# Optimization experiments

Hardware: AMD Instinct MI355X
Metric: run time of the kernel (lower is better)

Reference implementation:

```python
import jax, jax.numpy as jnp
import numpy as np

EMB = 1024
HID = 1536
NE = 8


def setup_inputs() -> dict:
    key = jax.random.key(0)
    ks = jax.random.split(key, 8)
    B, N, E, H, ne = 4, 2048, EMB, HID, NE
    s = 1.0 / np.sqrt(E)
    sh = 1.0 / np.sqrt(H)
    return {
        "x": jax.random.normal(ks[0], (B, N, E), dtype=jnp.float32),
        "Wr": jax.random.uniform(ks[1], (E, ne), minval=-s, maxval=s, dtype=jnp.float32),
        "br": jax.random.uniform(ks[2], (ne,), minval=-s, maxval=s, dtype=jnp.float32),
        "W1": jax.random.uniform(ks[3], (ne, E, H), minval=-s, maxval=s, dtype=jnp.float32),
        "b1": jax.random.uniform(ks[4], (ne, H), minval=-s, maxval=s, dtype=jnp.float32),
        "W2": jax.random.uniform(ks[5], (ne, H, E), minval=-sh, maxval=sh, dtype=jnp.float32),
        "b2": jax.random.uniform(ks[6], (ne, E), minval=-sh, maxval=sh, dtype=jnp.float32),
        "k": 2,
    }


def reference(x, Wr, br, W1, b1, W2, b2, k):
    B, N, E = x.shape
    T = B * N
    ne = Wr.shape[1]
    flat = x.reshape(T, E)
    logits = flat @ Wr + br                      # [T, ne]
    _, topk_idx = jax.lax.top_k(logits, k)       # [T, k]
    # counts[t, e] = number of top-k slots of token t assigned to expert e
    counts = jax.nn.one_hot(topk_idx, ne, dtype=flat.dtype).sum(axis=1)  # [T, ne]
    out = jnp.zeros_like(flat)
    for e in range(ne):  # small fixed loop over experts (structurally distinct weights)
        h = jax.nn.gelu(flat @ W1[e] + b1[e], approximate=False)  # torch nn.GELU = exact erf
        y = h @ W2[e] + b2[e]
        out = out + counts[:, e:e + 1] * y
    out = out / k
    return out.reshape(B, N, E)
```

## Files before the change

### kernel.cpp

```cpp
#include <hip/hip_runtime.h>
#include <hip/hip_bf16.h>
#include <math.h>

#define T_TOK 8192
#define EMB   1024
#define HID   1536
#define NE    8
#define NBINB 64
#define BINTOK (T_TOK / NBINB)

typedef float  floatx4 __attribute__((ext_vector_type(4)));
typedef __bf16 bf16x8  __attribute__((ext_vector_type(8)));

#define WS_COUNTS   0
#define WS_OFFSETS  1024
#define WS_FLAGS    2048
#define WS_BHIST    4096
#define WS_TOKMAP   8192
#define WS_TOKLIST  270336
#define WS_YBUF     532480
#define WS_W1T      34086912
#define WS_W2T      59252736
#define WS_H        84418560
#define WS_NEEDED   135143424

__device__ __forceinline__ float eload(const void* p, size_t idx, bool f32) {
  return f32 ? ((const float*)p)[idx] : (float)(((const __bf16*)p)[idx]);
}

__device__ __forceinline__ void glds16(const void* g, void* l) {
  __builtin_amdgcn_global_load_lds(
      (const __attribute__((address_space(1))) unsigned int*)g,
      (__attribute__((address_space(3))) unsigned int*)l, 16, 0, 0);
}

__global__ __launch_bounds__(256)
void sniff_kernel(const void* p0, const void* p1, const void* p2, const void* p3,
                  const void* p4, const void* p5, const void* p6, int* flags) {
  const void* ps[7] = {p0, p1, p2, p3, p4, p5, p6};
  const int nelem[7] = {T_TOK * EMB, EMB * NE, NE, NE * EMB * HID, NE * HID, NE * HID * EMB, NE * EMB};
  int t = blockIdx.x;
  const unsigned* w = (const unsigned*)ps[t];
  int nw = nelem[t] / 2;
  if (nw > 2048) nw = 2048;
  __shared__ int s_pl, s_nz;
  if (threadIdx.x == 0) { s_pl = 0; s_nz = 0; }
  __syncthreads();
  int pl = 0, nz = 0;
  for (int i = threadIdx.x; i < nw; i += 256) {
    unsigned v = w[i];
    if (v == 0) continue;
    nz++;
    unsigned e = (v >> 23) & 0xFF;
    if (e >= 100 && e <= 150) pl++;
  }
  atomicAdd(&s_pl, pl);
  atomicAdd(&s_nz, nz);
  __syncthreads();
  if (threadIdx.x == 0) flags[t] = (2 * s_pl > s_nz) ? 1 : 0;
}

__global__ __launch_bounds__(256)
void logits_kernel(const void* __restrict__ x, const void* __restrict__ Wr,
                   const void* __restrict__ br, const int* __restrict__ kptr,
                   const int* __restrict__ flags, int* __restrict__ topk,
                   __bf16* __restrict__ xbf) {
  const bool xf32  = flags[0] != 0;
  const bool wrf32 = flags[1] != 0;
  const bool brf32 = flags[2] != 0;
  const int wave = threadIdx.x >> 6;
  const int lane = threadIdx.x & 63;
  const int t = blockIdx.x * 4 + wave;

  float xv[16];
  {
    size_t base = (size_t)t * EMB + lane * 16;
    if (xf32) {
      const float* g = (const float*)x + base;
#pragma unroll
      for (int j = 0; j < 16; ++j) xv[j] = g[j];
    } else {
      bf16x8 u = *(const bf16x8*)((const __bf16*)x + base);
      bf16x8 v = *(const bf16x8*)((const __bf16*)x + base + 8);
#pragma unroll
      for (int j = 0; j < 8; ++j) { xv[j] = (float)u[j]; xv[8 + j] = (float)v[j]; }
    }
  }
  {
    bf16x8 o0, o1;
#pragma unroll
    for (int j = 0; j < 8; ++j) { o0[j] = (__bf16)xv[j]; o1[j] = (__bf16)xv[8 + j]; }
    __bf16* xo = xbf + (size_t)t * EMB + lane * 16;
    *(bf16x8*)xo = o0;
    *(bf16x8*)(xo + 8) = o1;
  }
  float acc[NE];
#pragma unroll
  for (int e = 0; e < NE; ++e) acc[e] = 0.f;
  if (wrf32) {
#pragma unroll
    for (int j = 0; j < 16; ++j) {
      const float* wr = (const float*)Wr + (size_t)(lane * 16 + j) * NE;
#pragma unroll
      for (int e = 0; e < NE; ++e) acc[e] += xv[j] * wr[e];
    }
  } else {
#pragma unroll
    for (int j = 0; j < 16; ++j) {
      bf16x8 wr = *(const bf16x8*)((const __bf16*)Wr + (size_t)(lane * 16 + j) * NE);
#pragma unroll
      for (int e = 0; e < NE; ++e) acc[e] += xv[j] * (float)wr[e];
    }
  }
#pragma unroll
  for (int e = 0; e < NE; ++e) {
#pragma unroll
    for (int off = 32; off > 0; off >>= 1)
      acc[e] += __shfl_xor(acc[e], off, 64);
  }
  if (lane == 0) {
    int k = kptr[0];
    if (k < 1) k = 1; if (k > NE) k = NE;
    float lg[NE];
#pragma unroll
    for (int e = 0; e < NE; ++e) lg[e] = acc[e] + eload(br, e, brf32);
    for (int s = 0; s < k; ++s) {
      int bi = 0; float bv = lg[0];
#pragma unroll
      for (int e = 1; e < NE; ++e) { if (lg[e] > bv) { bv = lg[e]; bi = e; } }
      lg[bi] = -3.0e38f;
      topk[t * 8 + s] = bi;
    }
  }
}

__global__ __launch_bounds__(128)
void bin1_kernel(const int* __restrict__ topk, const int* __restrict__ kptr,
                 int* __restrict__ bhist) {
  __shared__ int lhist[NE];
  if (threadIdx.x < NE) lhist[threadIdx.x] = 0;
  __syncthreads();
  int k = kptr[0];
  if (k < 1) k = 1; if (k > NE) k = NE;
  const int t = blockIdx.x * BINTOK + threadIdx.x;
  for (int s = 0; s < k; ++s) atomicAdd(&lhist[topk[t * 8 + s] & 7], 1);
  __syncthreads();
  if (threadIdx.x < NE) bhist[blockIdx.x * NE + threadIdx.x] = lhist[threadIdx.x];
}

__global__ __launch_bounds__(256)
void scan_kernel(int* __restrict__ bhist, int* __restrict__ counts, int* __restrict__ offsets) {
  __shared__ int sh[NBINB * NE];
  __shared__ int scnt[NE];
  __shared__ int soff[NE + 1];
  const int tid = threadIdx.x;
  for (int i = tid; i < NBINB * NE; i += 256) sh[i] = bhist[i];
  __syncthreads();
  if (tid < NE) {
    int s = 0;
    for (int b = 0; b < NBINB; ++b) s += sh[b * NE + tid];
    scnt[tid] = s;
  }
  __syncthreads();
  if (tid == 0) {
    int s = 0;
    for (int e = 0; e < NE; ++e) { soff[e] = s; s += scnt[e]; }
    soff[NE] = s;
  }
  __syncthreads();
  if (tid < NE) {
    int run = soff[tid];
    for (int b = 0; b < NBINB; ++b) {
      int v = sh[b * NE + tid];
      sh[b * NE + tid] = run;
      run += v;
    }
  }
  __syncthreads();
  for (int i = tid; i < NBINB * NE; i += 256) bhist[i] = sh[i];
  if (tid < NE) counts[tid] = scnt[tid];
  if (tid < NE + 1) offsets[tid] = soff[tid];
}

__global__ __launch_bounds__(128)
void bin2_kernel(const int* __restrict__ bhist, const int* __restrict__ offsets,
                 const int* __restrict__ kptr,
                 int* __restrict__ tok_list, int* __restrict__ tokmap) {
  __shared__ int lbase[NE];
  __shared__ int lcnt[NE];
  if (threadIdx.x < NE) {
    lbase[threadIdx.x] = bhist[blockIdx.x * NE + threadIdx.x];
    lcnt[threadIdx.x] = 0;
  }
  __syncthreads();
  int k = kptr[0];
  if (k < 1) k = 1; if (k > NE) k = NE;
  const int t = blockIdx.x * BINTOK + threadIdx.x;
  for (int s = 0; s < k; ++s) {
    int e = tokmap[t * 8 + s] & 7;
    int pos = atomicAdd(&lcnt[e], 1);
    int grow = lbase[e] + pos;
    tok_list[e * T_TOK + (grow - offsets[e])] = t;
    tokmap[t * 8 + s] = (e << 16) | grow;
  }
}

__global__ __launch_bounds__(256)
void transpose_kernel(const void* __restrict__ in, __bf16* __restrict__ out, int K, int N,
                      const int* __restrict__ flags, int fidx) {
  const bool f32 = flags[fidx] != 0;
  __shared__ __bf16 tile[64][65];
  size_t eoff = (size_t)blockIdx.z * (size_t)K * (size_t)N;
  int n0 = blockIdx.x * 64;
  int k0 = blockIdx.y * 64;
  int tx = threadIdx.x & 63;
  int ty = threadIdx.x >> 6;
#pragma unroll
  for (int i = 0; i < 16; ++i) {
    int r = i * 4 + ty;
    tile[r][tx] = (__bf16)eload(in, eoff + (size_t)(k0 + r) * N + (n0 + tx), f32);
  }
  __syncthreads();
#pragma unroll
  for (int i = 0; i < 16; ++i) {
    int r = i * 4 + ty;
    out[eoff + (size_t)(n0 + r) * K + (k0 + tx)] = tile[tx][r];
  }
}


#define STAGE3(SL, KO) do {                                              \
    __bf16* _d = lds + (SL) * 12288 + wave * 512;                        \
    glds16(pA0 + (KO), _d);                                              \
    glds16(pB0 + (KO), _d + 4096);                                       \
    glds16(pB1 + (KO), _d + 8192);                                       \
  } while (0)

#define KBODY(SL, DOSTAGE, TT) do {                                      \
    const char* _s = (const char*)lds + (SL) * 24576;                    \
    bf16x8 _af[4], _bf[4];                                               \
    _Pragma("unroll")                                                    \
    for (int _i = 0; _i < 4; ++_i) _af[_i] = *(const bf16x8*)(_s + aOff[_i]); \
    _Pragma("unroll")                                                    \
    for (int _j = 0; _j < 4; ++_j) _bf[_j] = *(const bf16x8*)(_s + bOff[_j]); \
    if (DOSTAGE) { int _sl2 = (SL) == 0 ? 2 : (SL) - 1;                  \
                   STAGE3(_sl2, (size_t)((TT) + 2) * 32); }              \
    __builtin_amdgcn_s_setprio(1);                                       \
    _Pragma("unroll")                                                    \
    for (int _i = 0; _i < 4; ++_i)                                       \
      _Pragma("unroll")                                                  \
      for (int _j = 0; _j < 4; ++_j)                                     \
        acc[_i][_j] = __builtin_amdgcn_mfma_f32_16x16x32_bf16(_af[_i], _bf[_j], acc[_i][_j], 0, 0, 0); \
    __builtin_amdgcn_s_setprio(0);                                       \
  } while (0)

__global__ __launch_bounds__(512, 4)
void gemm1_kernel(const __bf16* __restrict__ xbf, const __bf16* __restrict__ w1t,
                  const void* __restrict__ b1, const int* __restrict__ counts,
                  const int* __restrict__ offsets, const int* __restrict__ tok_list,
                  const int* __restrict__ flags, __bf16* __restrict__ hbuf) {
  const int flat = blockIdx.x;
  const int e   = flat & 7;
  const int idx = flat >> 3;
  const int g   = idx / 6;
  const int nT  = idx % 6;
  const int cnt = counts[e];
  const bool b1f32 = flags[4] != 0;

  __shared__ __align__(16) __bf16 lds[3 * 12288];

  const int wave = threadIdx.x >> 6;
  const int lane = threadIdx.x & 63;
  const int sr = wave * 16 + (lane >> 2);
  const int cg = (lane & 3) ^ ((sr >> 1) & 3);

  const __bf16* pB0 = w1t + ((size_t)e * HID + nT * 256 + sr) * EMB + cg * 8;
  const __bf16* pB1 = w1t + ((size_t)e * HID + nT * 256 + 128 + sr) * EMB + cg * 8;

  const int wm = (wave >> 2) * 64;
  const int wn = (wave & 3) * 64;
  const int fr = lane & 15;
  const int fc = lane >> 4;
  int aOff[4], bOff[4];
#pragma unroll
  for (int i = 0; i < 4; ++i) { int R = wm + i * 16 + fr; aOff[i] = R * 64 + ((fc ^ ((R >> 1) & 3)) << 4); }
#pragma unroll
  for (int j = 0; j < 4; ++j) { int R = wn + j * 16 + fr; bOff[j] = 8192 + R * 64 + ((fc ^ ((R >> 1) & 3)) << 4); }

  const int colBase = nT * 256 + wn + fr;
  float bv[4];
#pragma unroll
  for (int j = 0; j < 4; ++j) bv[j] = eload(b1, (size_t)e * HID + colBase + j * 16, b1f32);

  for (int mT = g; mT * 128 < cnt; mT += 16) {
    const int tokA = tok_list[e * T_TOK + mT * 128 + sr];
    const __bf16* pA0 = xbf + (size_t)tokA * EMB + cg * 8;

    floatx4 acc[4][4];
#pragma unroll
    for (int i = 0; i < 4; ++i)
#pragma unroll
      for (int j = 0; j < 4; ++j) acc[i][j] = (floatx4){0.f, 0.f, 0.f, 0.f};

    __syncthreads();
    STAGE3(0, 0); STAGE3(1, 32);
    int sl = 0;
    for (int t = 0; t < 31; ++t) {
      asm volatile("s_waitcnt vmcnt(3)" ::: "memory");
      __builtin_amdgcn_s_barrier();
      KBODY(sl, (t + 2 < 32), t);
      sl = (sl + 1 == 3) ? 0 : sl + 1;
    }
    asm volatile("s_waitcnt vmcnt(0)" ::: "memory");
    __builtin_amdgcn_s_barrier();
    KBODY(sl, 0, 0);

    const int hBase = offsets[e] + mT * 128;
#pragma unroll
    for (int i = 0; i < 4; ++i) {
      const int rowLoc = wm + i * 16 + fc * 4;
#pragma unroll
      for (int r = 0; r < 4; ++r) {
        const int row = rowLoc + r;
        if (mT * 128 + row < cnt) {
          __bf16* hp = hbuf + (size_t)(hBase + row) * HID + colBase;
#pragma unroll
          for (int j = 0; j < 4; ++j) {
            float v = acc[i][j][r] + bv[j];
            float gl = 0.5f * v * (1.0f + erff(v * 0.70710678118654752f));
            hp[j * 16] = (__bf16)gl;
          }
        }
      }
    }
  }
}

__global__ __launch_bounds__(512, 4)
void gemm2_kernel(const __bf16* __restrict__ hbuf, const __bf16* __restrict__ w2t,
                  const void* __restrict__ b2, const int* __restrict__ counts,
                  const int* __restrict__ offsets, const int* __restrict__ flags,
                  __bf16* __restrict__ ybuf) {
  const int flat = blockIdx.x;
  const int e   = flat & 7;
  const int idx = flat >> 3;
  const int g   = idx >> 2;
  const int nT  = idx & 3;
  const int cnt = counts[e];
  const bool b2f32 = flags[6] != 0;

  __shared__ __align__(16) __bf16 lds[3 * 12288];

  const int wave = threadIdx.x >> 6;
  const int lane = threadIdx.x & 63;
  const int sr = wave * 16 + (lane >> 2);
  const int cg = (lane & 3) ^ ((sr >> 1) & 3);

  const __bf16* pB0 = w2t + ((size_t)e * EMB + nT * 256 + sr) * HID + cg * 8;
  const __bf16* pB1 = w2t + ((size_t)e * EMB + nT * 256 + 128 + sr) * HID + cg * 8;

  const int wm = (wave >> 2) * 64;
  const int wn = (wave & 3) * 64;
  const int fr = lane & 15;
  const int fc = lane >> 4;
  int aOff[4], bOff[4];
#pragma unroll
  for (int i = 0; i < 4; ++i) { int R = wm + i * 16 + fr; aOff[i] = R * 64 + ((fc ^ ((R >> 1) & 3)) << 4); }
#pragma unroll
  for (int j = 0; j < 4; ++j) { int R = wn + j * 16 + fr; bOff[j] = 8192 + R * 64 + ((fc ^ ((R >> 1) & 3)) << 4); }

  const int colBase = nT * 256 + wn + fr;
  float bv[4];
#pragma unroll
  for (int j = 0; j < 4; ++j) bv[j] = eload(b2, (size_t)e * EMB + colBase + j * 16, b2f32);

  const int lastRow = offsets[NE] - 1;

  for (int mT = g; mT * 128 < cnt; mT += 16) {
    const int rowBase = offsets[e] + mT * 128;
    const int rA = min(rowBase + sr, lastRow);
    const __bf16* pA0 = hbuf + (size_t)rA * HID + cg * 8;

    floatx4 acc[4][4];
#pragma unroll
    for (int i = 0; i < 4; ++i)
#pragma unroll
      for (int j = 0; j < 4; ++j) acc[i][j] = (floatx4){0.f, 0.f, 0.f, 0.f};

    __syncthreads();
    STAGE3(0, 0); STAGE3(1, 32);
    int sl = 0;
    for (int t = 0; t < 47; ++t) {
      asm volatile("s_waitcnt vmcnt(3)" ::: "memory");
      __builtin_amdgcn_s_barrier();
      KBODY(sl, (t + 2 < 48), t);
      sl = (sl + 1 == 3) ? 0 : sl + 1;
    }
    asm volatile("s_waitcnt vmcnt(0)" ::: "memory");
    __builtin_amdgcn_s_barrier();
    KBODY(sl, 0, 0);

#pragma unroll
    for (int i = 0; i < 4; ++i) {
      const int rowLoc = wm + i * 16 + fc * 4;
#pragma unroll
      for (int r = 0; r < 4; ++r) {
        const int row = rowLoc + r;
        if (mT * 128 + row < cnt) {
          __bf16* yp = ybuf + (size_t)(rowBase + row) * EMB + colBase;
#pragma unroll
          for (int j = 0; j < 4; ++j)
            yp[j * 16] = (__bf16)(acc[i][j][r] + bv[j]);
        }
      }
    }
  }
}

__global__ __launch_bounds__(256)
void combine_kernel(const __bf16* __restrict__ ybuf, const int* __restrict__ tokmap,
                    const int* __restrict__ kptr, const int* __restrict__ flags,
                    void* __restrict__ out) {
  const bool f32 = flags[0] != 0;
  const int wave = threadIdx.x >> 6;
  const int lane = threadIdx.x & 63;
  const int t = blockIdx.x * 4 + wave;
  int k = kptr[0];
  if (k < 1) k = 1; if (k > NE) k = NE;
  const float invk = 1.0f / (float)k;
  int rows[NE];
  for (int s = 0; s < k; ++s) rows[s] = tokmap[t * 8 + s] & 0xFFFF;
#pragma unroll
  for (int c = 0; c < 2; ++c) {
    const int i = c * 512 + lane * 8;
    float a[8];
#pragma unroll
    for (int j = 0; j < 8; ++j) a[j] = 0.f;
    for (int s = 0; s < k; ++s) {
      bf16x8 y = *(const bf16x8*)(ybuf + (size_t)rows[s] * EMB + i);
#pragma unroll
      for (int j = 0; j < 8; ++j) a[j] += (float)y[j];
    }
    if (f32) {
      float* op = (float*)out + (size_t)t * EMB + i;
      float4 u = {a[0] * invk, a[1] * invk, a[2] * invk, a[3] * invk};
      float4 v = {a[4] * invk, a[5] * invk, a[6] * invk, a[7] * invk};
      *(float4*)op = u;
      *(float4*)(op + 4) = v;
    } else {
      bf16x8 o;
#pragma unroll
      for (int j = 0; j < 8; ++j) o[j] = (__bf16)(a[j] * invk);
      *(bf16x8*)((__bf16*)out + (size_t)t * EMB + i) = o;
    }
  }
}

extern "C" void kernel_launch(void* const* d_in, const int* in_sizes, int n_in,
                              void* d_out, int out_size, void* d_ws, size_t ws_size,
                              hipStream_t stream) {
  (void)in_sizes; (void)n_in; (void)out_size;
  if (ws_size < (size_t)WS_NEEDED) return;

  const void* x  = d_in[0];
  const void* Wr = d_in[1];
  const void* br = d_in[2];
  const void* W1 = d_in[3];
  const void* b1 = d_in[4];
  const void* W2 = d_in[5];
  const void* b2 = d_in[6];
  const int* kptr = (const int*)d_in[7];

  char* ws = (char*)d_ws;
  int*    counts   = (int*)(ws + WS_COUNTS);
  int*    offsets  = (int*)(ws + WS_OFFSETS);
  int*    flags    = (int*)(ws + WS_FLAGS);
  int*    bhist    = (int*)(ws + WS_BHIST);
  int*    tokmap   = (int*)(ws + WS_TOKMAP);
  int*    tok_list = (int*)(ws + WS_TOKLIST);
  __bf16* ybuf     = (__bf16*)(ws + WS_YBUF);
  __bf16* xbf      = (__bf16*)(ws + WS_YBUF);
  __bf16* w1t      = (__bf16*)(ws + WS_W1T);
  __bf16* w2t      = (__bf16*)(ws + WS_W2T);
  __bf16* hbuf     = (__bf16*)(ws + WS_H);

  hipMemsetAsync(ws, 0, WS_YBUF, stream);

  sniff_kernel<<<dim3(7), 256, 0, stream>>>(x, Wr, br, W1, b1, W2, b2, flags);

  transpose_kernel<<<dim3(HID / 64, EMB / 64, NE), 256, 0, stream>>>(W1, w1t, EMB, HID, flags, 3);
  transpose_kernel<<<dim3(EMB / 64, HID / 64, NE), 256, 0, stream>>>(W2, w2t, HID, EMB, flags, 5);

  logits_kernel<<<dim3(T_TOK / 4), 256, 0, stream>>>(x, Wr, br, kptr, flags, tokmap, xbf);
  bin1_kernel<<<dim3(NBINB), 128, 0, stream>>>(tokmap, kptr, bhist);
  scan_kernel<<<dim3(1), 256, 0, stream>>>(bhist, counts, offsets);
  bin2_kernel<<<dim3(NBINB), 128, 0, stream>>>(bhist, offsets, kptr, tok_list, tokmap);

  gemm1_kernel<<<dim3(8 * 16 * 6), 512, 0, stream>>>(
      xbf, w1t, b1, counts, offsets, tok_list, flags, hbuf);
  gemm2_kernel<<<dim3(8 * 16 * 4), 512, 0, stream>>>(
      hbuf, w2t, b2, counts, offsets, flags, ybuf);

  combine_kernel<<<dim3(T_TOK / 4), 256, 0, stream>>>(ybuf, tokmap, kptr, flags, d_out);
}
```

Baseline: 441.0 us.

## Replace pipelined 128x256 GEMM tiles with simple single-buffer 128x128 tiles

Both expert GEMMs drop the 3-stage LDS pipeline with 512-thread 128x256 tiles and use 256-thread 128x128 tiles that load and compute one K-slice per iteration between two barriers, doubling the grid. The two weight transposes are merged into one launch, and the memset shrinks to only the token list. The change loses load/compute overlap and halves the weight reuse per tile. gemm2 also drops the row clamp on A loads.

```diff
diff --git a/kernel.cpp b/kernel.cpp
--- a/kernel.cpp
+++ b/kernel.cpp
@@ -206,11 +206,16 @@
 }
 
 __global__ __launch_bounds__(256)
-void transpose_kernel(const void* __restrict__ in, __bf16* __restrict__ out, int K, int N,
-                      const int* __restrict__ flags, int fidx) {
-  const bool f32 = flags[fidx] != 0;
+void transpose2_kernel(const void* __restrict__ W1, const void* __restrict__ W2,
+                       __bf16* __restrict__ w1t, __bf16* __restrict__ w2t,
+                       const int* __restrict__ flags) {
+  const int z = blockIdx.z;
+  const void* in; __bf16* out; int K, N; bool f32;
+  if (z < 8) { in = W1; out = w1t; K = EMB; N = HID; f32 = flags[3] != 0; }
+  else       { in = W2; out = w2t; K = HID; N = EMB; f32 = flags[5] != 0; }
+  if ((int)blockIdx.x * 64 >= N || (int)blockIdx.y * 64 >= K) return;
   __shared__ __bf16 tile[64][65];
-  size_t eoff = (size_t)blockIdx.z * (size_t)K * (size_t)N;
+  size_t eoff = (size_t)(z & 7) * (size_t)K * (size_t)N;
   int n0 = blockIdx.x * 64;
   int k0 = blockIdx.y * 64;
   int tx = threadIdx.x & 63;
@@ -229,32 +234,7 @@
 }
 
 
-#define STAGE3(SL, KO) do {                                              \
-    __bf16* _d = lds + (SL) * 12288 + wave * 512;                        \
-    glds16(pA0 + (KO), _d);                                              \
-    glds16(pB0 + (KO), _d + 4096);                                       \
-    glds16(pB1 + (KO), _d + 8192);                                       \
-  } while (0)
-
-#define KBODY(SL, DOSTAGE, TT) do {                                      \
-    const char* _s = (const char*)lds + (SL) * 24576;                    \
-    bf16x8 _af[4], _bf[4];                                               \
-    _Pragma("unroll")                                                    \
-    for (int _i = 0; _i < 4; ++_i) _af[_i] = *(const bf16x8*)(_s + aOff[_i]); \
-    _Pragma("unroll")                                                    \
-    for (int _j = 0; _j < 4; ++_j) _bf[_j] = *(const bf16x8*)(_s + bOff[_j]); \
-    if (DOSTAGE) { int _sl2 = (SL) == 0 ? 2 : (SL) - 1;                  \
-                   STAGE3(_sl2, (size_t)((TT) + 2) * 32); }              \
-    __builtin_amdgcn_s_setprio(1);                                       \
-    _Pragma("unroll")                                                    \
-    for (int _i = 0; _i < 4; ++_i)                                       \
-      _Pragma("unroll")                                                  \
-      for (int _j = 0; _j < 4; ++_j)                                     \
-        acc[_i][_j] = __builtin_amdgcn_mfma_f32_16x16x32_bf16(_af[_i], _bf[_j], acc[_i][_j], 0, 0, 0); \
-    __builtin_amdgcn_s_setprio(0);                                       \
-  } while (0)
-
-__global__ __launch_bounds__(512, 4)
+__global__ __launch_bounds__(256, 4)
 void gemm1_kernel(const __bf16* __restrict__ xbf, const __bf16* __restrict__ w1t,
                   const void* __restrict__ b1, const int* __restrict__ counts,
                   const int* __restrict__ offsets, const int* __restrict__ tok_list,
@@ -262,39 +242,51 @@
   const int flat = blockIdx.x;
   const int e   = flat & 7;
   const int idx = flat >> 3;
-  const int g   = idx / 6;
-  const int nT  = idx % 6;
+  const int g   = idx / 12;
+  const int nT  = idx % 12;
   const int cnt = counts[e];
   const bool b1f32 = flags[4] != 0;
 
-  __shared__ __align__(16) __bf16 lds[3 * 12288];
+  __shared__ __align__(16) __bf16 As[128 * 32];
+  __shared__ __align__(16) __bf16 Bs[128 * 32];
 
   const int wave = threadIdx.x >> 6;
   const int lane = threadIdx.x & 63;
-  const int sr = wave * 16 + (lane >> 2);
-  const int cg = (lane & 3) ^ ((sr >> 1) & 3);
-
-  const __bf16* pB0 = w1t + ((size_t)e * HID + nT * 256 + sr) * EMB + cg * 8;
-  const __bf16* pB1 = w1t + ((size_t)e * HID + nT * 256 + 128 + sr) * EMB + cg * 8;
-
-  const int wm = (wave >> 2) * 64;
-  const int wn = (wave & 3) * 64;
+  const int sr = lane >> 2;
+  const int r0 = wave * 16 + sr;
+  const int r1 = 64 + wave * 16 + sr;
+  const int cg = (lane & 3) ^ ((r0 >> 1) & 3);
+
+  const __bf16* pB0base = w1t + ((size_t)e * HID + nT * 128 + r0) * EMB + cg * 8;
+  const __bf16* pB1base = w1t + ((size_t)e * HID + nT * 128 + r1) * EMB + cg * 8;
+
+  __bf16* dA0 = As + wave * 512;
+  __bf16* dA1 = As + 2048 + wave * 512;
+  __bf16* dB0 = Bs + wave * 512;
+  __bf16* dB1 = Bs + 2048 + wave * 512;
+
+  const int wm = (wave & 1) * 64;
+  const int wn = (wave >> 1) * 64;
   const int fr = lane & 15;
   const int fc = lane >> 4;
   int aOff[4], bOff[4];
 #pragma unroll
   for (int i = 0; i < 4; ++i) { int R = wm + i * 16 + fr; aOff[i] = R * 64 + ((fc ^ ((R >> 1) & 3)) << 4); }
 #pragma unroll
-  for (int j = 0; j < 4; ++j) { int R = wn + j * 16 + fr; bOff[j] = 8192 + R * 64 + ((fc ^ ((R >> 1) & 3)) << 4); }
-
-  const int colBase = nT * 256 + wn + fr;
+  for (int j = 0; j < 4; ++j) { int R = wn + j * 16 + fr; bOff[j] = R * 64 + ((fc ^ ((R >> 1) & 3)) << 4); }
+
+  const int colBase = nT * 128 + wn + fr;
   float bv[4];
 #pragma unroll
   for (int j = 0; j < 4; ++j) bv[j] = eload(b1, (size_t)e * HID + colBase + j * 16, b1f32);
 
   for (int mT = g; mT * 128 < cnt; mT += 16) {
-    const int tokA = tok_list[e * T_TOK + mT * 128 + sr];
-    const __bf16* pA0 = xbf + (size_t)tokA * EMB + cg * 8;
+    const int tokA0 = tok_list[e * T_TOK + mT * 128 + r0];
+    const int tokA1 = tok_list[e * T_TOK + mT * 128 + r1];
+    const __bf16* pA0 = xbf + (size_t)tokA0 * EMB + cg * 8;
+    const __bf16* pA1 = xbf + (size_t)tokA1 * EMB + cg * 8;
+    const __bf16* pB0 = pB0base;
+    const __bf16* pB1 = pB1base;
 
     floatx4 acc[4][4];
 #pragma unroll
@@ -302,18 +294,23 @@
 #pragma unroll
       for (int j = 0; j < 4; ++j) acc[i][j] = (floatx4){0.f, 0.f, 0.f, 0.f};
 
-    __syncthreads();
-    STAGE3(0, 0); STAGE3(1, 32);
-    int sl = 0;
-    for (int t = 0; t < 31; ++t) {
-      asm volatile("s_waitcnt vmcnt(3)" ::: "memory");
-      __builtin_amdgcn_s_barrier();
-      KBODY(sl, (t + 2 < 32), t);
-      sl = (sl + 1 == 3) ? 0 : sl + 1;
-    }
-    asm volatile("s_waitcnt vmcnt(0)" ::: "memory");
-    __builtin_amdgcn_s_barrier();
-    KBODY(sl, 0, 0);
+    for (int kb = 0; kb < EMB / 32; ++kb) {
+      __syncthreads();
+      glds16(pA0, dA0); glds16(pA1, dA1);
+      glds16(pB0, dB0); glds16(pB1, dB1);
+      pA0 += 32; pA1 += 32; pB0 += 32; pB1 += 32;
+      __syncthreads();
+      bf16x8 af[4], bfr[4];
+#pragma unroll
+      for (int i = 0; i < 4; ++i) af[i]  = *(const bf16x8*)((const char*)As + aOff[i]);
+#pragma unroll
+      for (int j = 0; j < 4; ++j) bfr[j] = *(const bf16x8*)((const char*)Bs + bOff[j]);
+#pragma unroll
+      for (int i = 0; i < 4; ++i)
+#pragma unroll
+        for (int j = 0; j < 4; ++j)
+          acc[i][j] = __builtin_amdgcn_mfma_f32_16x16x32_bf16(af[i], bfr[j], acc[i][j], 0, 0, 0);
+    }
 
     const int hBase = offsets[e] + mT * 128;
 #pragma unroll
@@ -336,7 +333,7 @@
   }
 }
 
-__global__ __launch_bounds__(512, 4)
+__global__ __launch_bounds__(256, 4)
 void gemm2_kernel(const __bf16* __restrict__ hbuf, const __bf16* __restrict__ w2t,
                   const void* __restrict__ b2, const int* __restrict__ counts,
                   const int* __restrict__ offsets, const int* __restrict__ flags,
@@ -344,42 +341,50 @@
   const int flat = blockIdx.x;
   const int e   = flat & 7;
   const int idx = flat >> 3;
-  const int g   = idx >> 2;
-  const int nT  = idx & 3;
+  const int g   = idx >> 3;
+  const int nT  = idx & 7;
   const int cnt = counts[e];
   const bool b2f32 = flags[6] != 0;
 
-  __shared__ __align__(16) __bf16 lds[3 * 12288];
+  __shared__ __align__(16) __bf16 As[128 * 32];
+  __shared__ __align__(16) __bf16 Bs[128 * 32];
 
   const int wave = threadIdx.x >> 6;
   const int lane = threadIdx.x & 63;
-  const int sr = wave * 16 + (lane >> 2);
-  const int cg = (lane & 3) ^ ((sr >> 1) & 3);
-
-  const __bf16* pB0 = w2t + ((size_t)e * EMB + nT * 256 + sr) * HID + cg * 8;
-  const __bf16* pB1 = w2t + ((size_t)e * EMB + nT * 256 + 128 + sr) * HID + cg * 8;
-
-  const int wm = (wave >> 2) * 64;
-  const int wn = (wave & 3) * 64;
+  const int sr = lane >> 2;
+  const int r0 = wave * 16 + sr;
+  const int r1 = 64 + wave * 16 + sr;
+  const int cg = (lane & 3) ^ ((r0 >> 1) & 3);
+
+  const __bf16* pB0base = w2t + ((size_t)e * EMB + nT * 128 + r0) * HID + cg * 8;
+  const __bf16* pB1base = w2t + ((size_t)e * EMB + nT * 128 + r1) * HID + cg * 8;
+
+  __bf16* dA0 = As + wave * 512;
+  __bf16* dA1 = As + 2048 + wave * 512;
+  __bf16* dB0 = Bs + wave * 512;
+  __bf16* dB1 = Bs + 2048 + wave * 512;
+
+  const int wm = (wave & 1) * 64;
+  const int wn = (wave >> 1) * 64;
   const int fr = lane & 15;
   const int fc = lane >> 4;
   int aOff[4], bOff[4];
 #pragma unroll
   for (int i = 0; i < 4; ++i) { int R = wm + i * 16 + fr; aOff[i] = R * 64 + ((fc ^ ((R >> 1) & 3)) << 4); }
 #pragma unroll
-  for (int j = 0; j < 4; ++j) { int R = wn + j * 16 + fr; bOff[j] = 8192 + R * 64 + ((fc ^ ((R >> 1) & 3)) << 4); }
-
-  const int colBase = nT * 256 + wn + fr;
+  for (int j = 0; j < 4; ++j) { int R = wn + j * 16 + fr; bOff[j] = R * 64 + ((fc ^ ((R >> 1) & 3)) << 4); }
+
+  const int colBase = nT * 128 + wn + fr;
   float bv[4];
 #pragma unroll
   for (int j = 0; j < 4; ++j) bv[j] = eload(b2, (size_t)e * EMB + colBase + j * 16, b2f32);
-
-  const int lastRow = offsets[NE] - 1;
 
   for (int mT = g; mT * 128 < cnt; mT += 16) {
     const int rowBase = offsets[e] + mT * 128;
-    const int rA = min(rowBase + sr, lastRow);
-    const __bf16* pA0 = hbuf + (size_t)rA * HID + cg * 8;
+    const __bf16* pA0 = hbuf + (size_t)(rowBase + r0) * HID + cg * 8;
+    const __bf16* pA1 = hbuf + (size_t)(rowBase + r1) * HID + cg * 8;
+    const __bf16* pB0 = pB0base;
+    const __bf16* pB1 = pB1base;
 
     floatx4 acc[4][4];
 #pragma unroll
@@ -387,18 +392,23 @@
 #pragma unroll
       for (int j = 0; j < 4; ++j) acc[i][j] = (floatx4){0.f, 0.f, 0.f, 0.f};
 
-    __syncthreads();
-    STAGE3(0, 0); STAGE3(1, 32);
-    int sl = 0;
-    for (int t = 0; t < 47; ++t) {
-      asm volatile("s_waitcnt vmcnt(3)" ::: "memory");
-      __builtin_amdgcn_s_barrier();
-      KBODY(sl, (t + 2 < 48), t);
-      sl = (sl + 1 == 3) ? 0 : sl + 1;
-    }
-    asm volatile("s_waitcnt vmcnt(0)" ::: "memory");
-    __builtin_amdgcn_s_barrier();
-    KBODY(sl, 0, 0);
+    for (int kb = 0; kb < HID / 32; ++kb) {
+      __syncthreads();
+      glds16(pA0, dA0); glds16(pA1, dA1);
+      glds16(pB0, dB0); glds16(pB1, dB1);
+      pA0 += 32; pA1 += 32; pB0 += 32; pB1 += 32;
+      __syncthreads();
+      bf16x8 af[4], bfr[4];
+#pragma unroll
+      for (int i = 0; i < 4; ++i) af[i]  = *(const bf16x8*)((const char*)As + aOff[i]);
+#pragma unroll
+      for (int j = 0; j < 4; ++j) bfr[j] = *(const bf16x8*)((const char*)Bs + bOff[j]);
+#pragma unroll
+      for (int i = 0; i < 4; ++i)
+#pragma unroll
+        for (int j = 0; j < 4; ++j)
+          acc[i][j] = __builtin_amdgcn_mfma_f32_16x16x32_bf16(af[i], bfr[j], acc[i][j], 0, 0, 0);
+    }
 
 #pragma unroll
     for (int i = 0; i < 4; ++i) {
@@ -484,21 +494,20 @@
   __bf16* w2t      = (__bf16*)(ws + WS_W2T);
   __bf16* hbuf     = (__bf16*)(ws + WS_H);
 
-  hipMemsetAsync(ws, 0, WS_YBUF, stream);
+  hipMemsetAsync(ws + WS_TOKLIST, 0, NE * T_TOK * 4, stream);
 
   sniff_kernel<<<dim3(7), 256, 0, stream>>>(x, Wr, br, W1, b1, W2, b2, flags);
 
-  transpose_kernel<<<dim3(HID / 64, EMB / 64, NE), 256, 0, stream>>>(W1, w1t, EMB, HID, flags, 3);
-  transpose_kernel<<<dim3(EMB / 64, HID / 64, NE), 256, 0, stream>>>(W2, w2t, HID, EMB, flags, 5);
+  transpose2_kernel<<<dim3(HID / 64, HID / 64, 16), 256, 0, stream>>>(W1, W2, w1t, w2t, flags);
 
   logits_kernel<<<dim3(T_TOK / 4), 256, 0, stream>>>(x, Wr, br, kptr, flags, tokmap, xbf);
   bin1_kernel<<<dim3(NBINB), 128, 0, stream>>>(tokmap, kptr, bhist);
   scan_kernel<<<dim3(1), 256, 0, stream>>>(bhist, counts, offsets);
   bin2_kernel<<<dim3(NBINB), 128, 0, stream>>>(bhist, offsets, kptr, tok_list, tokmap);
 
-  gemm1_kernel<<<dim3(8 * 16 * 6), 512, 0, stream>>>(
+  gemm1_kernel<<<dim3(8 * 16 * 12), 256, 0, stream>>>(
       xbf, w1t, b1, counts, offsets, tok_list, flags, hbuf);
-  gemm2_kernel<<<dim3(8 * 16 * 4), 512, 0, stream>>>(
+  gemm2_kernel<<<dim3(8 * 16 * 8), 256, 0, stream>>>(
       hbuf, w2t, b2, counts, offsets, flags, ybuf);
 
   combine_kernel<<<dim3(T_TOK / 4), 256, 0, stream>>>(ybuf, tokmap, kptr, flags, d_out);
```

Result: faster. 401.1 us (-9.0%).
